# Kernel tuning notes

Hardware: AMD Instinct MI355X
Metric: run time of the kernel (lower is better)

The kernel has to match this reference:

```python
import jax, jax.numpy as jnp
import numpy as np

B = 16        # number of lists
N = 1024      # items per list (all equal)
D = 256       # feature dim (= dim_emb, need_embedding=False)


def setup_inputs() -> dict:
    key = jax.random.key(0)
    k1, k2, k3 = jax.random.split(key, 3)
    feats = jax.random.normal(k1, (B * N, D), dtype=jnp.float32)
    length = jnp.full((B,), N, dtype=jnp.int32)
    # Bilinear params: torch nn.Bilinear(d, d, 1) -> weight [1, d, d], bias [1]
    # xavier_uniform on the 3-d weight: bound = sqrt(6 / (fan_in + fan_out)) with
    # fan_in = d (last dim), fan_out = 1*d (per torch _calculate_fan_in_and_fan_out)
    bound = float(np.sqrt(6.0 / (D + D)))
    W_upper = jax.random.uniform(k2, (1, D, D), jnp.float32, -bound, bound)
    W_lower = jax.random.uniform(k3, (1, D, D), jnp.float32, -bound, bound)
    b_upper = jnp.zeros((1,), jnp.float32)
    b_lower = jnp.zeros((1,), jnp.float32)
    return {"feats": feats, "W_upper": W_upper, "b_upper": b_upper,
            "W_lower": W_lower, "b_lower": b_lower, "length": length}


def reference(feats, W_upper, b_upper, W_lower, b_lower, length):
    # nb_layers=0, need_embedding=False -> embedding and transformer are Identity.
    b = length.shape[0]
    n = feats.shape[0] // b  # equal-length lists -> static reshape
    d = feats.shape[-1]
    X = feats.reshape(b, n, d)  # [B, n, d]
    # For list i: repeated_feats_1 row (p*n + q) = x_p, repeated_feats_2 row = x_q,
    # so adjacency[p, q] = x_p^T W x_q + bias  (Bilinear with out=1).
    upper = jnp.einsum('bnd,de,bme->bnm', X, W_upper[0], X) + b_upper[0]
    lower = jnp.einsum('bnd,de,bme->bnm', X, W_lower[0], X) + b_lower[0]
    adj = jnp.triu(upper) + jnp.tril(lower, -1)  # [B, n, n]
    return adj
```

## Files before the change

### kernel.cpp

```cpp
#include <hip/hip_runtime.h>

#define BL 16
#define NL 1024
#define DD 256

typedef short bf16x8 __attribute__((ext_vector_type(8)));
typedef float f32x4 __attribute__((ext_vector_type(4)));

static __device__ __forceinline__ short f32_to_bf16(float f) {
  union { float f; unsigned u; } v; v.f = f;
  unsigned r = (v.u + 0x7FFFu + ((v.u >> 16) & 1u)) >> 16;
  return (short)r;
}

static __device__ __forceinline__ void g2l16(const short* g, short* l) {
  __builtin_amdgcn_global_load_lds(
      (const __attribute__((address_space(1))) void*)g,
      (__attribute__((address_space(3))) void*)l, 16, 0, 0);
}

__global__ __launch_bounds__(256) void k_prep(const float* __restrict__ X,
                                              const float* __restrict__ Wu,
                                              const float* __restrict__ Wl,
                                              short* __restrict__ Xb,
                                              short* __restrict__ WTu,
                                              short* __restrict__ WTl) {
  const int bid = blockIdx.x;
  if (bid < 4096) {
    int i = bid * 256 + threadIdx.x;
    const float4 v = ((const float4*)X)[i];
    short4 o;
    o.x = f32_to_bf16(v.x); o.y = f32_to_bf16(v.y);
    o.z = f32_to_bf16(v.z); o.w = f32_to_bf16(v.w);
    ((short4*)Xb)[i] = o;
  } else {
    const int id = bid - 4096;
    const int z = id >> 8, d = id & 255;
    const float* W = z ? Wl : Wu;
    short* WT = z ? WTl : WTu;
    const int e = threadIdx.x;
    WT[e * DD + d] = f32_to_bf16(W[d * DD + e]);
  }
}

__global__ __launch_bounds__(1024, 4) void k_fused(const short* __restrict__ Xb,
                                                   const short* __restrict__ WTu,
                                                   const short* __restrict__ WTl,
                                                   const float* __restrict__ bu_p,
                                                   const float* __restrict__ bl_p,
                                                   float* __restrict__ out) {
  __shared__ short Asw[64 * 256];
  __shared__ short Yu[64 * 256];
  __shared__ short Yl[64 * 256];

  const int bid = blockIdx.x;
  const int b = bid & 15, pt = bid >> 4;
  const int t = threadIdx.x, lane = t & 63, w = t >> 6;
  const int r = lane & 15, quad = lane >> 4;
  const size_t listoff = (size_t)b * NL * DD;
  const short* Ap = Xb + listoff + (size_t)pt * 64 * DD;

#pragma unroll
  for (int i = 0; i < 2; ++i) {
    const int c = i * 1024 + t;
    const int src = c ^ ((c >> 5) & 7);
    g2l16(Ap + src * 8, Asw + c * 8);
  }
  __syncthreads();

  {
    const int n0 = w * 16;
    f32x4 aU[4] = {}, aL[4] = {};
#pragma unroll
    for (int ks = 0; ks < 8; ++ks) {
      bf16x8 af[4];
#pragma unroll
      for (int mt = 0; mt < 4; ++mt) {
        const int row = mt * 16 + r;
        const int abyte = (row * 512 + ks * 64 + quad * 16) ^ ((row & 7) << 4);
        af[mt] = *(const bf16x8*)((const char*)Asw + abyte);
      }
      const int off = (n0 + r) * DD + ks * 32 + quad * 8;
      const bf16x8 bfu = *(const bf16x8*)(WTu + off);
      const bf16x8 bfl = *(const bf16x8*)(WTl + off);
#pragma unroll
      for (int mt = 0; mt < 4; ++mt) {
        aU[mt] = __builtin_amdgcn_mfma_f32_16x16x32_bf16(af[mt], bfu, aU[mt], 0, 0, 0);
        aL[mt] = __builtin_amdgcn_mfma_f32_16x16x32_bf16(af[mt], bfl, aL[mt], 0, 0, 0);
      }
    }
#pragma unroll
    for (int mt = 0; mt < 4; ++mt)
#pragma unroll
      for (int i = 0; i < 4; ++i) {
        const int row = mt * 16 + quad * 4 + i;
        const int col = n0 + r;
        const int byte = (row * 512 + col * 2) ^ ((row & 7) << 4);
        *(short*)((char*)Yu + byte) = f32_to_bf16(aU[mt][i]);
        *(short*)((char*)Yl + byte) = f32_to_bf16(aL[mt][i]);
      }
  }
  __syncthreads();

  const float ub = bu_p[0], lb = bl_p[0];
  float* Ob = out + (size_t)b * NL * NL;
  const int p0 = pt * 64;
  const int qt = w, q0 = qt * 64;
  const short* Bg = Xb + listoff + (size_t)qt * 64 * DD;
  const short* YA = (qt >= pt) ? Yu : Yl;
  const float bias = (qt >= pt) ? ub : lb;

  f32x4 acc[4][4] = {};
#pragma unroll
  for (int ks = 0; ks < 8; ++ks) {
    bf16x8 af[4], bf[4];
#pragma unroll
    for (int mt = 0; mt < 4; ++mt) {
      const int row = mt * 16 + r;
      const int abyte = (row * 512 + ks * 64 + quad * 16) ^ ((row & 7) << 4);
      af[mt] = *(const bf16x8*)((const char*)YA + abyte);
    }
#pragma unroll
    for (int nt = 0; nt < 4; ++nt)
      bf[nt] = *(const bf16x8*)(Bg + (size_t)(nt * 16 + r) * DD + ks * 32 + quad * 8);
#pragma unroll
    for (int nt = 0; nt < 4; ++nt)
#pragma unroll
      for (int mt = 0; mt < 4; ++mt)
        acc[nt][mt] = __builtin_amdgcn_mfma_f32_16x16x32_bf16(bf[nt], af[mt],
                                                              acc[nt][mt], 0, 0, 0);
  }
#pragma unroll
  for (int mt = 0; mt < 4; ++mt) {
    float* row = Ob + (size_t)(p0 + mt * 16 + r) * NL;
#pragma unroll
    for (int nt = 0; nt < 4; ++nt) {
      f32x4 v;
#pragma unroll
      for (int i = 0; i < 4; ++i) v[i] = acc[nt][mt][i] + bias;
      *(f32x4*)(row + q0 + nt * 16 + quad * 4) = v;
    }
  }

  if (qt == pt) {
    f32x4 accL[4][4] = {};
#pragma unroll
    for (int ks = 0; ks < 8; ++ks) {
      bf16x8 af[4], bf[4];
#pragma unroll
      for (int mt = 0; mt < 4; ++mt) {
        const int row = mt * 16 + r;
        const int abyte = (row * 512 + ks * 64 + quad * 16) ^ ((row & 7) << 4);
        af[mt] = *(const bf16x8*)((const char*)Yl + abyte);
      }
#pragma unroll
      for (int nt = 0; nt < 4; ++nt)
        bf[nt] = *(const bf16x8*)(Bg + (size_t)(nt * 16 + r) * DD + ks * 32 + quad * 8);
#pragma unroll
      for (int nt = 0; nt < 4; ++nt)
#pragma unroll
        for (int mt = 0; mt < 4; ++mt)
          accL[nt][mt] = __builtin_amdgcn_mfma_f32_16x16x32_bf16(bf[nt], af[mt],
                                                                 accL[nt][mt], 0, 0, 0);
    }
#pragma unroll
    for (int mt = 0; mt < 4; ++mt) {
      const int p = p0 + mt * 16 + r;
      float* row = Ob + (size_t)p * NL;
#pragma unroll
      for (int nt = 0; nt < 4; ++nt)
#pragma unroll
        for (int i = 0; i < 4; ++i) {
          const int q = q0 + nt * 16 + quad * 4 + i;
          if (q < p) row[q] = accL[nt][mt][i] + lb;
        }
    }
  }
}

extern "C" void kernel_launch(void* const* d_in, const int* in_sizes, int n_in,
                              void* d_out, int out_size, void* d_ws, size_t ws_size,
                              hipStream_t stream) {
  const float* feats = (const float*)d_in[0];
  const float* Wu    = (const float*)d_in[1];
  const float* bu    = (const float*)d_in[2];
  const float* Wl    = (const float*)d_in[3];
  const float* bl    = (const float*)d_in[4];
  float* out = (float*)d_out;

  char* ws = (char*)d_ws;
  short* Xb  = (short*)(ws);
  short* WTu = (short*)(ws + (size_t)8 * 1024 * 1024);
  short* WTl = (short*)(ws + (size_t)8 * 1024 * 1024 + DD * DD * 2);

  k_prep<<<4096 + 512, 256, 0, stream>>>(feats, Wu, Wl, Xb, WTu, WTl);

  k_fused<<<256, 1024, 0, stream>>>(Xb, WTu, WTl, bu, bl, out);
}
```

Baseline: 130.5 us.

## Enlarge row tile to 128, merge diagonal outputs, stage stores through LDS

Each block now handles 128 rows of P and half of the Q columns. The per-block projection X·W therefore covers 128 rows and is shared by 16 waves, reusing the W loads over twice as many rows. The shared buffers are reused, with Yl overwriting the A tile after a barrier. Diagonal tiles now merge the upper and lower results in registers, replacing the scalar masked stores. All output is transposed through LDS scratch so each row is written with fully coalesced 16-byte stores. The cost is that the projection is computed twice per 128-row tile, once for each q-half, along with extra barriers and LDS traffic.

```diff
diff --git a/kernel.cpp b/kernel.cpp
--- a/kernel.cpp
+++ b/kernel.cpp
@@ -49,66 +49,72 @@
                                                    const float* __restrict__ bu_p,
                                                    const float* __restrict__ bl_p,
                                                    float* __restrict__ out) {
-  __shared__ short Asw[64 * 256];
-  __shared__ short Yu[64 * 256];
-  __shared__ short Yl[64 * 256];
+  __shared__ short BufL[128 * 256];
+  __shared__ short BufU[128 * 256];
 
   const int bid = blockIdx.x;
-  const int b = bid & 15, pt = bid >> 4;
+  const int b = bid & 15, z = bid >> 4;
+  const int pt = z >> 1, qh = z & 1;
   const int t = threadIdx.x, lane = t & 63, w = t >> 6;
   const int r = lane & 15, quad = lane >> 4;
   const size_t listoff = (size_t)b * NL * DD;
-  const short* Ap = Xb + listoff + (size_t)pt * 64 * DD;
-
-#pragma unroll
-  for (int i = 0; i < 2; ++i) {
+  const short* Ap = Xb + listoff + (size_t)pt * 128 * DD;
+
+#pragma unroll
+  for (int i = 0; i < 4; ++i) {
     const int c = i * 1024 + t;
     const int src = c ^ ((c >> 5) & 7);
-    g2l16(Ap + src * 8, Asw + c * 8);
-  }
-  __syncthreads();
-
-  {
-    const int n0 = w * 16;
-    f32x4 aU[4] = {}, aL[4] = {};
-#pragma unroll
-    for (int ks = 0; ks < 8; ++ks) {
-      bf16x8 af[4];
-#pragma unroll
-      for (int mt = 0; mt < 4; ++mt) {
-        const int row = mt * 16 + r;
-        const int abyte = (row * 512 + ks * 64 + quad * 16) ^ ((row & 7) << 4);
-        af[mt] = *(const bf16x8*)((const char*)Asw + abyte);
-      }
-      const int off = (n0 + r) * DD + ks * 32 + quad * 8;
-      const bf16x8 bfu = *(const bf16x8*)(WTu + off);
-      const bf16x8 bfl = *(const bf16x8*)(WTl + off);
-#pragma unroll
-      for (int mt = 0; mt < 4; ++mt) {
-        aU[mt] = __builtin_amdgcn_mfma_f32_16x16x32_bf16(af[mt], bfu, aU[mt], 0, 0, 0);
-        aL[mt] = __builtin_amdgcn_mfma_f32_16x16x32_bf16(af[mt], bfl, aL[mt], 0, 0, 0);
-      }
-    }
-#pragma unroll
-    for (int mt = 0; mt < 4; ++mt)
-#pragma unroll
-      for (int i = 0; i < 4; ++i) {
-        const int row = mt * 16 + quad * 4 + i;
-        const int col = n0 + r;
-        const int byte = (row * 512 + col * 2) ^ ((row & 7) << 4);
-        *(short*)((char*)Yu + byte) = f32_to_bf16(aU[mt][i]);
-        *(short*)((char*)Yl + byte) = f32_to_bf16(aL[mt][i]);
-      }
-  }
+    g2l16(Ap + src * 8, BufL + c * 8);
+  }
+  __syncthreads();
+
+  const int n0 = w * 16;
+  f32x4 aU[8] = {}, aL[8] = {};
+#pragma unroll
+  for (int ks = 0; ks < 8; ++ks) {
+    bf16x8 af[8];
+#pragma unroll
+    for (int mt = 0; mt < 8; ++mt) {
+      const int row = mt * 16 + r;
+      const int abyte = (row * 512 + ks * 64 + quad * 16) ^ ((row & 7) << 4);
+      af[mt] = *(const bf16x8*)((const char*)BufL + abyte);
+    }
+    const int off = (n0 + r) * DD + ks * 32 + quad * 8;
+    const bf16x8 bfu = *(const bf16x8*)(WTu + off);
+    const bf16x8 bfl = *(const bf16x8*)(WTl + off);
+#pragma unroll
+    for (int mt = 0; mt < 8; ++mt) {
+      aU[mt] = __builtin_amdgcn_mfma_f32_16x16x32_bf16(af[mt], bfu, aU[mt], 0, 0, 0);
+      aL[mt] = __builtin_amdgcn_mfma_f32_16x16x32_bf16(af[mt], bfl, aL[mt], 0, 0, 0);
+    }
+  }
+#pragma unroll
+  for (int mt = 0; mt < 8; ++mt)
+#pragma unroll
+    for (int i = 0; i < 4; ++i) {
+      const int row = mt * 16 + quad * 4 + i;
+      const int byte = (row * 512 + (n0 + r) * 2) ^ ((row & 7) << 4);
+      *(short*)((char*)BufU + byte) = f32_to_bf16(aU[mt][i]);
+    }
+  __syncthreads();
+#pragma unroll
+  for (int mt = 0; mt < 8; ++mt)
+#pragma unroll
+    for (int i = 0; i < 4; ++i) {
+      const int row = mt * 16 + quad * 4 + i;
+      const int byte = (row * 512 + (n0 + r) * 2) ^ ((row & 7) << 4);
+      *(short*)((char*)BufL + byte) = f32_to_bf16(aL[mt][i]);
+    }
   __syncthreads();
 
   const float ub = bu_p[0], lb = bl_p[0];
-  float* Ob = out + (size_t)b * NL * NL;
-  const int p0 = pt * 64;
-  const int qt = w, q0 = qt * 64;
+  const int h = w >> 3, j = w & 7;
+  const int p0 = pt * 128 + h * 64;
+  const int qt = qh * 8 + j, q0 = qt * 64;
   const short* Bg = Xb + listoff + (size_t)qt * 64 * DD;
-  const short* YA = (qt >= pt) ? Yu : Yl;
-  const float bias = (qt >= pt) ? ub : lb;
+  const bool upper = (q0 >= p0);
+  const short* YA = upper ? BufU : BufL;
+  const int rbase = h * 64;
 
   f32x4 acc[4][4] = {};
 #pragma unroll
@@ -116,7 +122,7 @@
     bf16x8 af[4], bf[4];
 #pragma unroll
     for (int mt = 0; mt < 4; ++mt) {
-      const int row = mt * 16 + r;
+      const int row = rbase + mt * 16 + r;
       const int abyte = (row * 512 + ks * 64 + quad * 16) ^ ((row & 7) << 4);
       af[mt] = *(const bf16x8*)((const char*)YA + abyte);
     }
@@ -130,28 +136,18 @@
         acc[nt][mt] = __builtin_amdgcn_mfma_f32_16x16x32_bf16(bf[nt], af[mt],
                                                               acc[nt][mt], 0, 0, 0);
   }
-#pragma unroll
-  for (int mt = 0; mt < 4; ++mt) {
-    float* row = Ob + (size_t)(p0 + mt * 16 + r) * NL;
-#pragma unroll
-    for (int nt = 0; nt < 4; ++nt) {
-      f32x4 v;
-#pragma unroll
-      for (int i = 0; i < 4; ++i) v[i] = acc[nt][mt][i] + bias;
-      *(f32x4*)(row + q0 + nt * 16 + quad * 4) = v;
-    }
-  }
-
-  if (qt == pt) {
+
+  float bias = upper ? ub : lb;
+  if (q0 == p0) {
     f32x4 accL[4][4] = {};
 #pragma unroll
     for (int ks = 0; ks < 8; ++ks) {
       bf16x8 af[4], bf[4];
 #pragma unroll
       for (int mt = 0; mt < 4; ++mt) {
-        const int row = mt * 16 + r;
+        const int row = rbase + mt * 16 + r;
         const int abyte = (row * 512 + ks * 64 + quad * 16) ^ ((row & 7) << 4);
-        af[mt] = *(const bf16x8*)((const char*)Yl + abyte);
+        af[mt] = *(const bf16x8*)((const char*)BufL + abyte);
       }
 #pragma unroll
       for (int nt = 0; nt < 4; ++nt)
@@ -164,16 +160,37 @@
                                                                  accL[nt][mt], 0, 0, 0);
     }
 #pragma unroll
-    for (int mt = 0; mt < 4; ++mt) {
-      const int p = p0 + mt * 16 + r;
-      float* row = Ob + (size_t)p * NL;
-#pragma unroll
-      for (int nt = 0; nt < 4; ++nt)
+    for (int nt = 0; nt < 4; ++nt)
+#pragma unroll
+      for (int mt = 0; mt < 4; ++mt)
 #pragma unroll
         for (int i = 0; i < 4; ++i) {
           const int q = q0 + nt * 16 + quad * 4 + i;
-          if (q < p) row[q] = accL[nt][mt][i] + lb;
+          const int p = p0 + mt * 16 + r;
+          acc[nt][mt][i] = (q >= p) ? acc[nt][mt][i] + ub : accL[nt][mt][i] + lb;
         }
+    bias = 0.f;
+  }
+
+  __syncthreads();
+  float* scr = (float*)BufL + w * 1024;
+  float* Ob = out + (size_t)b * NL * NL;
+#pragma unroll
+  for (int mt = 0; mt < 4; ++mt) {
+#pragma unroll
+    for (int nt = 0; nt < 4; ++nt) {
+      f32x4 v;
+#pragma unroll
+      for (int i = 0; i < 4; ++i) v[i] = acc[nt][mt][i] + bias;
+      const int sb = (r * 256 + nt * 64 + quad * 16) ^ ((r & 7) << 4);
+      *(f32x4*)((char*)scr + sb) = v;
+    }
+#pragma unroll
+    for (int k = 0; k < 4; ++k) {
+      const int row = k * 4 + quad;
+      const int rb = (row * 256 + r * 16) ^ ((row & 7) << 4);
+      const f32x4 v = *(const f32x4*)((const char*)scr + rb);
+      *(f32x4*)(Ob + (size_t)(p0 + mt * 16 + row) * NL + q0 + r * 4) = v;
     }
   }
 }
```

Result: slower. 164.5 us (+26.1%).

## Restructure second GEMM stage with double-buffered LDS X tiles and per-wave 16x16 outputs

Applied to the files above, without the earlier changes.

Stage two previously had each wave read its 64-row X tile straight from global memory and compute a full 64x64 output tile, then run an extra lower-matrix pass on the diagonal tile. Now all 16 waves share one X tile, which is streamed into LDS with async global-to-LDS loads into two alternating buffers. The waves iterate over the 16 column tiles, each computing one 16x16 sub-block for both upper and lower using A fragments held in registers, and they pick between upper and lower per element. This removes repeated global reads and the diagonal divergence, but adds per-tile barriers, manual vmcnt waits, and more LDS (64KB → 64KB+, 4 buffers of 32KB = 128KB) which may cut occupancy.

```diff
diff --git a/kernel.cpp b/kernel.cpp
--- a/kernel.cpp
+++ b/kernel.cpp
@@ -49,9 +49,10 @@
                                                    const float* __restrict__ bu_p,
                                                    const float* __restrict__ bl_p,
                                                    float* __restrict__ out) {
-  __shared__ short Asw[64 * 256];
   __shared__ short Yu[64 * 256];
   __shared__ short Yl[64 * 256];
+  __shared__ short Bb0[64 * 256];
+  __shared__ short Bb1[64 * 256];
 
   const int bid = blockIdx.x;
   const int b = bid & 15, pt = bid >> 4;
@@ -59,12 +60,13 @@
   const int r = lane & 15, quad = lane >> 4;
   const size_t listoff = (size_t)b * NL * DD;
   const short* Ap = Xb + listoff + (size_t)pt * 64 * DD;
+  const float ub = bu_p[0], lb = bl_p[0];
 
 #pragma unroll
   for (int i = 0; i < 2; ++i) {
-    const int c = i * 1024 + t;
-    const int src = c ^ ((c >> 5) & 7);
-    g2l16(Ap + src * 8, Asw + c * 8);
+    const int c16 = i * 1024 + t;
+    const int src = c16 ^ ((c16 >> 5) & 7);
+    g2l16(Ap + src * 8, Bb0 + c16 * 8);
   }
   __syncthreads();
 
@@ -78,7 +80,7 @@
       for (int mt = 0; mt < 4; ++mt) {
         const int row = mt * 16 + r;
         const int abyte = (row * 512 + ks * 64 + quad * 16) ^ ((row & 7) << 4);
-        af[mt] = *(const bf16x8*)((const char*)Asw + abyte);
+        af[mt] = *(const bf16x8*)((const char*)Bb0 + abyte);
       }
       const int off = (n0 + r) * DD + ks * 32 + quad * 8;
       const bf16x8 bfu = *(const bf16x8*)(WTu + off);
@@ -94,86 +96,83 @@
 #pragma unroll
       for (int i = 0; i < 4; ++i) {
         const int row = mt * 16 + quad * 4 + i;
-        const int col = n0 + r;
-        const int byte = (row * 512 + col * 2) ^ ((row & 7) << 4);
+        const int byte = (row * 512 + (n0 + r) * 2) ^ ((row & 7) << 4);
         *(short*)((char*)Yu + byte) = f32_to_bf16(aU[mt][i]);
         *(short*)((char*)Yl + byte) = f32_to_bf16(aL[mt][i]);
       }
   }
   __syncthreads();
 
-  const float ub = bu_p[0], lb = bl_p[0];
-  float* Ob = out + (size_t)b * NL * NL;
-  const int p0 = pt * 64;
-  const int qt = w, q0 = qt * 64;
-  const short* Bg = Xb + listoff + (size_t)qt * 64 * DD;
-  const short* YA = (qt >= pt) ? Yu : Yl;
-  const float bias = (qt >= pt) ? ub : lb;
+  const short* Bl = Xb + listoff;
+#pragma unroll
+  for (int i = 0; i < 2; ++i) {
+    const int c16 = i * 1024 + t;
+    const int src = c16 ^ ((c16 >> 5) & 7);
+    g2l16(Bl + src * 8, Bb0 + c16 * 8);
+  }
 
-  f32x4 acc[4][4] = {};
+  const int pg = w >> 2, qg = w & 3;
+  const int prow = pg * 16 + r;
+  bf16x8 afU[8], afL[8];
 #pragma unroll
   for (int ks = 0; ks < 8; ++ks) {
-    bf16x8 af[4], bf[4];
-#pragma unroll
-    for (int mt = 0; mt < 4; ++mt) {
-      const int row = mt * 16 + r;
-      const int abyte = (row * 512 + ks * 64 + quad * 16) ^ ((row & 7) << 4);
-      af[mt] = *(const bf16x8*)((const char*)YA + abyte);
-    }
-#pragma unroll
-    for (int nt = 0; nt < 4; ++nt)
-      bf[nt] = *(const bf16x8*)(Bg + (size_t)(nt * 16 + r) * DD + ks * 32 + quad * 8);
-#pragma unroll
-    for (int nt = 0; nt < 4; ++nt)
-#pragma unroll
-      for (int mt = 0; mt < 4; ++mt)
-        acc[nt][mt] = __builtin_amdgcn_mfma_f32_16x16x32_bf16(bf[nt], af[mt],
-                                                              acc[nt][mt], 0, 0, 0);
-  }
-#pragma unroll
-  for (int mt = 0; mt < 4; ++mt) {
-    float* row = Ob + (size_t)(p0 + mt * 16 + r) * NL;
-#pragma unroll
-    for (int nt = 0; nt < 4; ++nt) {
-      f32x4 v;
-#pragma unroll
-      for (int i = 0; i < 4; ++i) v[i] = acc[nt][mt][i] + bias;
-      *(f32x4*)(row + q0 + nt * 16 + quad * 4) = v;
-    }
+    const int abyte = (prow * 512 + ks * 64 + quad * 16) ^ ((prow & 7) << 4);
+    afU[ks] = *(const bf16x8*)((const char*)Yu + abyte);
+    afL[ks] = *(const bf16x8*)((const char*)Yl + abyte);
   }
 
-  if (qt == pt) {
-    f32x4 accL[4][4] = {};
+  float* Ob = out + (size_t)b * NL * NL;
+  const int p = pt * 64 + pg * 16 + r;
+  const int qrow = qg * 16 + r;
+  float* const prowp = Ob + (size_t)p * NL;
+
+#pragma unroll
+  for (int c = 0; c < 16; ++c) {
+    if (c + 1 < 16) {
+      const short* Bgn = Bl + (size_t)(c + 1) * 64 * DD;
+      short* dst = ((c + 1) & 1) ? Bb1 : Bb0;
+#pragma unroll
+      for (int i = 0; i < 2; ++i) {
+        const int c16 = i * 1024 + t;
+        const int src = c16 ^ ((c16 >> 5) & 7);
+        g2l16(Bgn + src * 8, dst + c16 * 8);
+      }
+    }
+    if (c == 0)       asm volatile("s_waitcnt vmcnt(2)" ::: "memory");
+    else if (c == 15) asm volatile("s_waitcnt vmcnt(1)" ::: "memory");
+    else              asm volatile("s_waitcnt vmcnt(3)" ::: "memory");
+    __builtin_amdgcn_sched_barrier(0);
+    __builtin_amdgcn_s_barrier();
+    __builtin_amdgcn_sched_barrier(0);
+
+    const short* Bc = (c & 1) ? Bb1 : Bb0;
+    f32x4 accU = {}, accL = {};
 #pragma unroll
     for (int ks = 0; ks < 8; ++ks) {
-      bf16x8 af[4], bf[4];
+      const int bbyte = (qrow * 512 + ks * 64 + quad * 16) ^ ((qrow & 7) << 4);
+      const bf16x8 bf = *(const bf16x8*)((const char*)Bc + bbyte);
+      accU = __builtin_amdgcn_mfma_f32_16x16x32_bf16(bf, afU[ks], accU, 0, 0, 0);
+      accL = __builtin_amdgcn_mfma_f32_16x16x32_bf16(bf, afL[ks], accL, 0, 0, 0);
+    }
+    const int qb = c * 64 + qg * 16 + quad * 4;
+    f32x4 v;
+    if (c > pt) {
 #pragma unroll
-      for (int mt = 0; mt < 4; ++mt) {
-        const int row = mt * 16 + r;
-        const int abyte = (row * 512 + ks * 64 + quad * 16) ^ ((row & 7) << 4);
-        af[mt] = *(const bf16x8*)((const char*)Yl + abyte);
-      }
+      for (int i = 0; i < 4; ++i) v[i] = accU[i] + ub;
+    } else if (c < pt) {
 #pragma unroll
-      for (int nt = 0; nt < 4; ++nt)
-        bf[nt] = *(const bf16x8*)(Bg + (size_t)(nt * 16 + r) * DD + ks * 32 + quad * 8);
+      for (int i = 0; i < 4; ++i) v[i] = accL[i] + lb;
+    } else {
 #pragma unroll
-      for (int nt = 0; nt < 4; ++nt)
-#pragma unroll
-        for (int mt = 0; mt < 4; ++mt)
-          accL[nt][mt] = __builtin_amdgcn_mfma_f32_16x16x32_bf16(bf[nt], af[mt],
-                                                                 accL[nt][mt], 0, 0, 0);
+      for (int i = 0; i < 4; ++i)
+        v[i] = (qb + i >= p) ? accU[i] + ub : accL[i] + lb;
     }
-#pragma unroll
-    for (int mt = 0; mt < 4; ++mt) {
-      const int p = p0 + mt * 16 + r;
-      float* row = Ob + (size_t)p * NL;
-#pragma unroll
-      for (int nt = 0; nt < 4; ++nt)
-#pragma unroll
-        for (int i = 0; i < 4; ++i) {
-          const int q = q0 + nt * 16 + quad * 4 + i;
-          if (q < p) row[q] = accL[nt][mt][i] + lb;
-        }
+    *(f32x4*)(prowp + qb) = v;
+
+    if (c + 1 < 16) {
+      __builtin_amdgcn_sched_barrier(0);
+      __builtin_amdgcn_s_barrier();
+      __builtin_amdgcn_sched_barrier(0);
     }
   }
 }
```

New measurement: 115.7 us. 1.13x faster.
